# Kernel optimization log

Hardware: AMD Instinct MI355X
Metric: run time of the kernel (lower is better)

Reference implementation:

```python
import jax, jax.numpy as jnp
import numpy as np

V = 32000   # vocab
E = 512     # hidden_size (d_model)
NH = 8      # num_heads
DH = E // NH
NL = 2      # num_layers
FF = 2048   # TransformerDecoderLayer default dim_feedforward
MAXLEN = 24 # cfg.max_length -> gen_len (no target given)
S, B = 48, 8
TRANS = 14
INIT = TRANS - 2            # tgt = transform[1:-1]
LF = INIT + MAXLEN - 1      # final tgt length after the loop
EPS = 1e-5
NEG = -1e9


def pos_encoding(length, d):
    pos = np.arange(length, dtype=np.float32)[:, None]
    div = np.exp(-np.log(10000.0) * np.arange(0, d, 2, dtype=np.float32) / d)
    pe = np.zeros((length, d), dtype=np.float32)
    pe[:, 0::2] = np.sin(pos * div)
    pe[:, 1::2] = np.cos(pos * div)
    return jnp.asarray(pe)


def setup_inputs() -> dict:
    key = jax.random.key(0)
    ks = jax.random.split(key, 12)
    s = 0.02
    return {
        "enc_outputs": jax.random.normal(ks[0], (S, B, E), jnp.float32),
        "transform": jax.random.randint(ks[1], (TRANS, B), 0, V),
        "tf_ratio": 0,
        "emb_table": jax.random.normal(ks[2], (V, E), jnp.float32) * s,
        "sa_w": jax.random.normal(ks[3], (NL, 3 * E, E), jnp.float32) * s,
        "sa_b": jnp.zeros((NL, 3 * E), jnp.float32),
        "sa_ow": jax.random.normal(ks[4], (NL, E, E), jnp.float32) * s,
        "sa_ob": jnp.zeros((NL, E), jnp.float32),
        "ca_w": jax.random.normal(ks[5], (NL, 3 * E, E), jnp.float32) * s,
        "ca_b": jnp.zeros((NL, 3 * E), jnp.float32),
        "ca_ow": jax.random.normal(ks[6], (NL, E, E), jnp.float32) * s,
        "ca_ob": jnp.zeros((NL, E), jnp.float32),
        "ff1_w": jax.random.normal(ks[7], (NL, FF, E), jnp.float32) * s,
        "ff1_b": jnp.zeros((NL, FF), jnp.float32),
        "ff2_w": jax.random.normal(ks[8], (NL, E, FF), jnp.float32) * s,
        "ff2_b": jnp.zeros((NL, E), jnp.float32),
        "ln_g": jnp.ones((NL, 3, E), jnp.float32),
        "ln_b": jnp.zeros((NL, 3, E), jnp.float32),
        "out_w": jax.random.normal(ks[9], (V, E), jnp.float32) * s,
        "out_b": jnp.zeros((V,), jnp.float32),
    }


def _ln(x, g, b):
    m = jnp.mean(x, -1, keepdims=True)
    v = jnp.mean((x - m) ** 2, -1, keepdims=True)
    return (x - m) * jax.lax.rsqrt(v + EPS) * g + b


def _mha(q_in, kv_in, w, b, ow, ob, mask):
    # q_in [Lq,B,E], kv_in [Lk,B,E]; PyTorch packed in_proj [3E,E]
    wq, wk, wv = jnp.split(w, 3, 0)
    bq, bk, bv = jnp.split(b, 3, 0)
    proj = lambda x, wm, bm: (x @ wm.T + bm).reshape(x.shape[0], x.shape[1], NH, DH)
    q, k, v = proj(q_in, wq, bq), proj(kv_in, wk, bk), proj(kv_in, wv, bv)
    sc = jnp.einsum('qbhd,kbhd->bhqk', q, k) / np.sqrt(DH).astype(np.float32)
    if mask is not None:
        sc = sc + mask
    a = jax.nn.softmax(sc, -1)
    o = jnp.einsum('bhqk,kbhd->qbhd', a, v).reshape(q_in.shape[0], q_in.shape[1], E)
    return o @ ow.T + ob


def _decoder(x, mem, mask, p):
    # post-norm TransformerDecoderLayer: self-attn -> cross-attn -> relu FFN
    for l in range(NL):
        x = _ln(x + _mha(x, x, p['sa_w'][l], p['sa_b'][l], p['sa_ow'][l], p['sa_ob'][l], mask),
                p['ln_g'][l, 0], p['ln_b'][l, 0])
        x = _ln(x + _mha(x, mem, p['ca_w'][l], p['ca_b'][l], p['ca_ow'][l], p['ca_ob'][l], None),
                p['ln_g'][l, 1], p['ln_b'][l, 1])
        h = jax.nn.relu(x @ p['ff1_w'][l].T + p['ff1_b'][l]) @ p['ff2_w'][l].T + p['ff2_b'][l]
        x = _ln(x + h, p['ln_g'][l, 2], p['ln_b'][l, 2])
    return x


def reference(enc_outputs, transform, tf_ratio, emb_table, sa_w, sa_b, sa_ow, sa_ob,
              ca_w, ca_b, ca_ow, ca_ob, ff1_w, ff1_b, ff2_w, ff2_b, ln_g, ln_b,
              out_w, out_b):
    # tf_ratio == 0 -> no teacher forcing; gen_len = max_length (no target attr)
    p = dict(sa_w=sa_w, sa_b=sa_b, sa_ow=sa_ow, sa_ob=sa_ob, ca_w=ca_w, ca_b=ca_b,
             ca_ow=ca_ow, ca_ob=ca_ob, ff1_w=ff1_w, ff1_b=ff1_b, ff2_w=ff2_w,
             ff2_b=ff2_b, ln_g=ln_g, ln_b=ln_b)
    pe = pos_encoding(MAXLEN, E)
    # causal mask over the fixed-size buffer; padded (future) slots cannot
    # influence valid positions, so full-buffer passes == torch prefix passes.
    mask = jnp.where(jnp.tril(jnp.ones((LF, LF), bool)), 0.0, NEG)
    tgt0 = emb_table[transform[1:-1]] + pe[:INIT][:, None, :]   # [INIT,B,E]
    buf = jnp.zeros((LF, B, E), jnp.float32).at[:INIT].set(tgt0)

    def step(buf, i):
        h = _decoder(buf, enc_outputs, mask, p)
        pos = INIT - 1 + i                        # last valid position
        pred = jnp.argmax(h[pos] @ out_w.T + out_b, axis=-1)   # [B]
        # torch re-embeds the single predicted token -> PE position 0
        emb = emb_table[pred] + pe[0]
        return buf.at[pos + 1].set(emb), None

    buf, _ = jax.lax.scan(step, buf, jnp.arange(MAXLEN - 1))
    h = _decoder(buf, enc_outputs, mask, p)       # final loop iteration's pass
    return h @ out_w.T + out_b                    # dec_outputs [LF,B,V]
```

## Files before the change

### kernel.cpp

```cpp
#include <hip/hip_runtime.h>
#include <hip/hip_bf16.h>
#include <math.h>

#define V    32000
#define E    512
#define NH   8
#define DH   64
#define NL   2
#define FF   2048
#define MAXLEN 24
#define S    48
#define B    8
#define TRANS 14
#define INIT 12
#define LF   35

#define NB   256
#define NT   512

typedef float f4 __attribute__((ext_vector_type(4)));

__device__ inline float wsum(float v) {
#pragma unroll
  for (int off = 32; off; off >>= 1) v += __shfl_xor(v, off);
  return v;
}
__device__ inline float wmax(float v) {
#pragma unroll
  for (int off = 32; off; off >>= 1) v = fmaxf(v, __shfl_xor(v, off));
  return v;
}

__device__ inline float ldc(const float* p) {
  return __hip_atomic_load(p, __ATOMIC_RELAXED, __HIP_MEMORY_SCOPE_AGENT);
}
__device__ inline void stc(float* p, float v) {
  __hip_atomic_store(p, v, __ATOMIC_RELAXED, __HIP_MEMORY_SCOPE_AGENT);
}
__device__ inline float2 ldc8(const float* p) {
  union { unsigned long long u; float2 f; } c;
  c.u = __hip_atomic_load((const unsigned long long*)p, __ATOMIC_RELAXED, __HIP_MEMORY_SCOPE_AGENT);
  return c.f;
}
__device__ inline void stc8(float* p, float x, float y) {
  union { unsigned long long u; float f[2]; } c; c.f[0] = x; c.f[1] = y;
  __hip_atomic_store((unsigned long long*)p, c.u, __ATOMIC_RELAXED, __HIP_MEMORY_SCOPE_AGENT);
}
__device__ inline int ldci(const int* p) {
  return __hip_atomic_load(p, __ATOMIC_RELAXED, __HIP_MEMORY_SCOPE_AGENT);
}
__device__ inline void stci(int* p, int v) {
  __hip_atomic_store(p, v, __ATOMIC_RELAXED, __HIP_MEMORY_SCOPE_AGENT);
}

#define CMB(v, idx, ov, oi) do { if ((ov) > (v) || ((ov) == (v) && (oi) < (idx))) { (v) = (ov); (idx) = (oi); } } while (0)


__global__ void embed_init_k(const int* __restrict__ transform, const float* __restrict__ emb,
                             float* __restrict__ xbuf) {
  int t = blockIdx.x;
  int pos = t >> 3, b = t & 7;
  int tok = transform[(1 + pos) * B + b];
  for (int d = threadIdx.x; d < E; d += blockDim.x) {
    double div = exp(-log(10000.0) * (double)(d & ~1) / (double)E);
    double ang = (double)pos * div;
    float pe = (d & 1) ? (float)cos(ang) : (float)sin(ang);
    xbuf[(size_t)t * E + d] = emb[(size_t)tok * E + d] + pe;
  }
}

template <int K>
__global__ __launch_bounds__(256) void gemm_k(
    const float* __restrict__ x, const float* __restrict__ W, const float* __restrict__ bias,
    int ntok, int nout, int route, int relu,
    float* __restrict__ out0, float* __restrict__ out1, float* __restrict__ out2) {
  constexpr int K4 = K / 4;
  constexpr int J  = K / 256;
  __shared__ float4 xt[8][K4];
  const int tid = threadIdx.x;
  const int lane = tid & 63;
  const int o = blockIdx.x * 4 + (tid >> 6);

  float4 wr[J];
  if (o < nout) {
    const float4* Wr = (const float4*)(W + (size_t)o * K);
#pragma unroll
    for (int j = 0; j < J; ++j) wr[j] = Wr[lane + 64 * j];
  }

  const int ng = ntok >> 3;
  for (int g = 0; g < ng; ++g) {
    if (g) __syncthreads();
    const float4* xg = (const float4*)(x + (size_t)g * 8 * K);
    float4* xf = &xt[0][0];
    for (int i = tid; i < 8 * K4; i += 256) xf[i] = xg[i];
    __syncthreads();
    if (o < nout) {
      float acc[8] = {0, 0, 0, 0, 0, 0, 0, 0};
#pragma unroll
      for (int j = 0; j < J; ++j) {
        float4 w = wr[j];
#pragma unroll
        for (int tt = 0; tt < 8; ++tt) {
          float4 xv = xt[tt][lane + 64 * j];
          acc[tt] += w.x * xv.x + w.y * xv.y + w.z * xv.z + w.w * xv.w;
        }
      }
#pragma unroll
      for (int tt = 0; tt < 8; ++tt) acc[tt] = wsum(acc[tt]);
      if (lane == 0) {
        float bo = bias[o];
#pragma unroll
        for (int tt = 0; tt < 8; ++tt) {
          float v = acc[tt] + bo;
          if (relu) v = fmaxf(v, 0.f);
          int t = g * 8 + tt;
          if (route == 0) {
            out0[(size_t)t * nout + o] = v;
          } else if (route == 1) {
            if (o < E) out0[(size_t)t * E + o] = v;
            else if (o < 2 * E) out1[(size_t)t * E + (o - E)] = v;
            else out2[(size_t)t * E + (o - 2 * E)] = v;
          } else {
            if (o < E) out0[(size_t)t * E + o] = v;
            else out1[(size_t)t * E + (o - E)] = v;
          }
        }
      }
    }
  }
}

__global__ __launch_bounds__(256) void attn_k(
    const float* __restrict__ q, const float* __restrict__ Kc, const float* __restrict__ Vc,
    float* __restrict__ outp, int p0, int nq, int nk_fixed, int causal) {
  const int tid = threadIdx.x;
  const int lane = tid & 63;
  const int u = blockIdx.x * 4 + (tid >> 6);
  if (u >= nq * 64) return;
  const int qi = u >> 6;
  const int r = u & 63;
  const int b = r >> 3, h = r & 7;
  const int nk = causal ? (p0 + qi + 1) : nk_fixed;

  const size_t qoff = (size_t)(qi * B + b) * E + h * DH + lane;
  const float qv = q[qoff];

  float myscore = -INFINITY;
  for (int k = 0; k < nk; ++k) {
    float prod = qv * Kc[(size_t)(k * B + b) * E + h * DH + lane];
    prod = wsum(prod);
    if (lane == k) myscore = prod * 0.125f;
  }
  float m = wmax(myscore);
  float p = (lane < nk) ? expf(myscore - m) : 0.f;
  float denom = wsum(p);
  float a = p / denom;

  float oacc = 0.f;
  for (int k = 0; k < nk; ++k) {
    float ak = __shfl(a, k);
    oacc = fmaf(ak, Vc[(size_t)(k * B + b) * E + h * DH + lane], oacc);
  }
  outp[qoff] = oacc;
}

__global__ __launch_bounds__(256) void add_ln_k(
    const float* __restrict__ xa, const float* __restrict__ xb,
    const float* __restrict__ g, const float* __restrict__ beta,
    float* __restrict__ outp, int ntok) {
  const int tid = threadIdx.x, lane = tid & 63;
  const int t = blockIdx.x * 4 + (tid >> 6);
  if (t >= ntok) return;
  float v[8];
  float s = 0.f;
#pragma unroll
  for (int j = 0; j < 8; ++j) {
    int d = lane + 64 * j;
    v[j] = xa[(size_t)t * E + d] + xb[(size_t)t * E + d];
    s += v[j];
  }
  s = wsum(s);
  float mean = s * (1.f / 512.f);
  float d2 = 0.f;
#pragma unroll
  for (int j = 0; j < 8; ++j) { float dd = v[j] - mean; d2 += dd * dd; }
  d2 = wsum(d2);
  float inv = 1.f / sqrtf(d2 * (1.f / 512.f) + 1e-5f);
#pragma unroll
  for (int j = 0; j < 8; ++j) {
    int d = lane + 64 * j;
    outp[(size_t)t * E + d] = (v[j] - mean) * inv * g[d] + beta[d];
  }
}


__global__ __launch_bounds__(NT, 1) void decode_persist_k(
    const float* __restrict__ emb,
    const float* __restrict__ sa_w, const float* __restrict__ sa_b,
    const float* __restrict__ sa_ow, const float* __restrict__ sa_ob,
    const float* __restrict__ ca_w, const float* __restrict__ ca_b,
    const float* __restrict__ ca_ow, const float* __restrict__ ca_ob,
    const float* __restrict__ ff1_w, const float* __restrict__ ff1_b,
    const float* __restrict__ ff2_w, const float* __restrict__ ff2_b,
    const float* __restrict__ ln_g, const float* __restrict__ ln_b,
    const float* __restrict__ out_w, const float* __restrict__ out_b,
    float* __restrict__ kself, float* __restrict__ vself,
    const float* __restrict__ kcross, const float* __restrict__ vcross,
    float* __restrict__ x3buf, float* __restrict__ xstep, float* __restrict__ part,
    float* __restrict__ amaxbuf, float* __restrict__ outp, int* __restrict__ bar) {
  __shared__ __align__(16) float s_x[E];
  __shared__ __align__(16) float s_q[DH];
  __shared__ __align__(16) float s_att[DH];
  __shared__ __align__(16) float s_h[256];
  __shared__ __align__(16) float s_tile[8 * E];
  __shared__ float s_rv[NT];
  __shared__ int   s_ri[NT];
  __shared__ float s_r1[8], s_r2[8];
  __shared__ float s_pv[8][8];
  __shared__ int   s_pi[8][8];

  const int tid  = threadIdx.x;
  const int lane = tid & 63;
  const int wv   = tid >> 6;
  const int g4   = lane >> 2;
  const int s4   = lane & 3;
  const int bid  = blockIdx.x;
  const int b    = bid >> 3;
  const int j    = bid & 7;

  int cgen = 0;

  auto cl_sync = [&]() {
    ++cgen;
    __syncthreads();
    if (tid == 0) {
      __hip_atomic_fetch_add(&bar[b * 32], 1, __ATOMIC_RELAXED, __HIP_MEMORY_SCOPE_AGENT);
      while (ldci(&bar[b * 32]) < 8 * cgen) __builtin_amdgcn_s_sleep(2);
    }
    __syncthreads();
  };

  auto dot512 = [&](const float* Wrow, const float* xin) -> float {
    const f4* Wp = (const f4*)Wrow;
    const f4* Xp = (const f4*)xin;
    float acc = 0.f;
#pragma unroll
    for (int u = 0; u < 32; ++u) {
      int jj = s4 * 32 + ((u + s4) & 31);
      f4 w = Wp[jj], x = Xp[jj];
      acc += w.x * x.x + w.y * x.y + w.z * x.z + w.w * x.w;
    }
    acc += __shfl_xor(acc, 1);
    acc += __shfl_xor(acc, 2);
    return acc;
  };
  auto dot256 = [&](const float* Wseg, const float* xin) -> float {
    const f4* Wp = (const f4*)Wseg;
    const f4* Xp = (const f4*)xin;
    float acc = 0.f;
#pragma unroll
    for (int u = 0; u < 16; ++u) {
      int jj = s4 * 16 + ((u + s4) & 15);
      f4 w = Wp[jj], x = Xp[jj];
      acc += w.x * x.x + w.y * x.y + w.z * x.z + w.w * x.w;
    }
    acc += __shfl_xor(acc, 1);
    acc += __shfl_xor(acc, 2);
    return acc;
  };
  auto dot64 = [&](const float* Wseg, const float* xin) -> float {
    const f4* Wp = (const f4*)Wseg;
    const f4* Xp = (const f4*)xin;
    float acc = 0.f;
#pragma unroll
    for (int u = 0; u < 4; ++u) {
      int jj = s4 * 4 + ((u + s4) & 3);
      f4 w = Wp[jj], x = Xp[jj];
      acc += w.x * x.x + w.y * x.y + w.z * x.z + w.w * x.w;
    }
    acc += __shfl_xor(acc, 1);
    acc += __shfl_xor(acc, 2);
    return acc;
  };

  auto blockLN = [&](float val, const float* gg, const float* be, float* dst) {
    float s1 = wsum(val);
    if (lane == 0) s_r1[wv] = s1;
    __syncthreads();
    float m = 0.f;
#pragma unroll
    for (int w2 = 0; w2 < 8; ++w2) m += s_r1[w2];
    m *= (1.f / 512.f);
    float d = val - m;
    float s2 = wsum(d * d);
    if (lane == 0) s_r2[wv] = s2;
    __syncthreads();
    float var = 0.f;
#pragma unroll
    for (int w2 = 0; w2 < 8; ++w2) var += s_r2[w2];
    var *= (1.f / 512.f);
    float inv = 1.f / sqrtf(var + 1e-5f);
    dst[tid] = d * inv * gg[tid] + be[tid];
    __syncthreads();
  };

  auto attn1 = [&](const float* Kbase, const float* Vbase, int nk) {
    if (wv == 0) {
      float sc = -INFINITY;
      if (lane < nk) {
        const f4* Kr = (const f4*)(Kbase + ((size_t)lane * B + b) * E + j * DH);
        const f4* Qp = (const f4*)s_q;
        float a0 = 0.f;
#pragma unroll
        for (int u = 0; u < 16; ++u) {
          f4 kv = Kr[u], qv = Qp[u];
          a0 += kv.x * qv.x + kv.y * qv.y + kv.z * qv.z + kv.w * qv.w;
        }
        sc = a0 * 0.125f;
      }
      float m = wmax(sc);
      float e = (lane < nk) ? expf(sc - m) : 0.f;
      float den = wsum(e);
      float aa = e / den;
      float o = 0.f;
      for (int k2 = 0; k2 < nk; ++k2) {
        float ak = __shfl(aa, k2);
        o = fmaf(ak, Vbase[((size_t)k2 * B + b) * E + j * DH + lane], o);
      }
      s_att[lane] = o;
    }
    __syncthreads();
  };

  for (int i = 0; i < MAXLEN - 1; ++i) {
    const int p = INIT + i;

    if (bid < 64) {
      if (j == 0) {
        if (i > 0) {
          if (tid < 32) {
            while (ldci(&bar[(18 + tid) * 32]) < 8 * i) __builtin_amdgcn_s_sleep(4);
          }
          __syncthreads();
          if (tid < 256) {
            float2 pr = ldc8(&amaxbuf[(size_t)(tid * 8 + b) * 2]);
            s_rv[tid] = pr.x; s_ri[tid] = (int)pr.y;
          } else { s_rv[tid] = -INFINITY; s_ri[tid] = 0x7fffffff; }
          __syncthreads();
          for (int st2 = 128; st2; st2 >>= 1) {
            if (tid < st2) {
              float ov = s_rv[tid + st2]; int oi = s_ri[tid + st2];
              CMB(s_rv[tid], s_ri[tid], ov, oi);
            }
            __syncthreads();
          }
        } else {
          const float* row = outp + ((size_t)(INIT - 1) * B + b) * V;
          float bv = -INFINITY; int bi = 0x7fffffff;
          for (int j2 = tid; j2 < V / 2; j2 += NT) {
            float2 vv = ldc8(row + 2 * j2);
            CMB(bv, bi, vv.x, 2 * j2);
            CMB(bv, bi, vv.y, 2 * j2 + 1);
          }
          s_rv[tid] = bv; s_ri[tid] = bi;
          __syncthreads();
          for (int st2 = NT / 2; st2; st2 >>= 1) {
            if (tid < st2) {
              float ov = s_rv[tid + st2]; int oi = s_ri[tid + st2];
              CMB(s_rv[tid], s_ri[tid], ov, oi);
            }
            __syncthreads();
          }
        }
        const int tok = s_ri[0];
        if (tid < 256) {
          int d0 = tid * 2;
          float e0 = emb[(size_t)tok * E + d0];
          float e1 = emb[(size_t)tok * E + d0 + 1] + 1.0f;
          s_x[d0] = e0; s_x[d0 + 1] = e1;
          stc8(&xstep[(size_t)b * E + d0], e0, e1);
        }
        __syncthreads();
        if (tid == 0) stci(&bar[(10 + b) * 32], i + 1);
      } else {
        if (tid == 0) {
          while (ldci(&bar[(10 + b) * 32]) < i + 1) __builtin_amdgcn_s_sleep(4);
        }
        __syncthreads();
        if (tid < 256) {
          float2 vv = ldc8(&xstep[(size_t)b * E + tid * 2]);
          s_x[tid * 2] = vv.x; s_x[tid * 2 + 1] = vv.y;
        }
        __syncthreads();
      }

      for (int l = 0; l < NL; ++l) {
        for (int c = wv; c < 12; c += 8) {
          int r = c * 16 + g4;
          int sec = r >> 6, off = r & 63;
          int wr = sec * E + j * DH + off;
          float val = dot512(sa_w + ((size_t)l * 3 * E + wr) * E, s_x);
          if (s4 == 0) {
            val += sa_b[(size_t)l * 3 * E + wr];
            if (sec == 0) s_q[off] = val;
            else if (sec == 1) kself[((size_t)(l * LF + p) * B + b) * E + j * DH + off] = val;
            else               vself[((size_t)(l * LF + p) * B + b) * E + j * DH + off] = val;
          }
        }
        __syncthreads();
        attn1(kself + (size_t)l * LF * B * E, vself + (size_t)l * LF * B * E, p + 1);
        for (int ps = 0; ps < 4; ++ps) {
          int r = wv * 64 + ps * 16 + g4;
          float val = dot64(sa_ow + ((size_t)l * E + r) * E + j * DH, s_att);
          if (s4 == 0) stc(&part[(((size_t)(l * 3 + 0) * 8 + b) * 8 + j) * E + r], val);
        }
        cl_sync();
        {
          float val = s_x[tid] + sa_ob[(size_t)l * E + tid];
          const float* pb = part + ((size_t)(l * 3 + 0) * 8 + b) * 8 * E + tid;
#pragma unroll
          for (int jj = 0; jj < 8; ++jj) val += ldc(pb + jj * E);
          blockLN(val, ln_g + (size_t)(l * 3 + 0) * E, ln_b + (size_t)(l * 3 + 0) * E, s_x);
        }
        if (wv < 4) {
          int r = wv * 16 + g4;
          float val = dot512(ca_w + ((size_t)l * 3 * E + j * DH + r) * E, s_x);
          if (s4 == 0) s_q[r] = val + ca_b[(size_t)l * 3 * E + j * DH + r];
        }
        __syncthreads();
        attn1(kcross + (size_t)l * S * B * E, vcross + (size_t)l * S * B * E, S);
        for (int ps = 0; ps < 4; ++ps) {
          int r = wv * 64 + ps * 16 + g4;
          float val = dot64(ca_ow + ((size_t)l * E + r) * E + j * DH, s_att);
          if (s4 == 0) stc(&part[(((size_t)(l * 3 + 1) * 8 + b) * 8 + j) * E + r], val);
        }
        cl_sync();
        {
          float val = s_x[tid] + ca_ob[(size_t)l * E + tid];
          const float* pb = part + ((size_t)(l * 3 + 1) * 8 + b) * 8 * E + tid;
#pragma unroll
          for (int jj = 0; jj < 8; ++jj) val += ldc(pb + jj * E);
          blockLN(val, ln_g + (size_t)(l * 3 + 1) * E, ln_b + (size_t)(l * 3 + 1) * E, s_x);
        }
        for (int c = wv; c < 16; c += 8) {
          int r = c * 16 + g4;
          int wr = j * 256 + r;
          float val = dot512(ff1_w + ((size_t)l * FF + wr) * E, s_x);
          if (s4 == 0) s_h[r] = fmaxf(val + ff1_b[(size_t)l * FF + wr], 0.f);
        }
        __syncthreads();
        for (int ps = 0; ps < 4; ++ps) {
          int r = wv * 64 + ps * 16 + g4;
          float val = dot256(ff2_w + ((size_t)l * E + r) * FF + j * 256, s_h);
          if (s4 == 0) stc(&part[(((size_t)(l * 3 + 2) * 8 + b) * 8 + j) * E + r], val);
        }
        cl_sync();
        {
          float val = s_x[tid] + ff2_b[(size_t)l * E + tid];
          const float* pb = part + ((size_t)(l * 3 + 2) * 8 + b) * 8 * E + tid;
#pragma unroll
          for (int jj = 0; jj < 8; ++jj) val += ldc(pb + jj * E);
          blockLN(val, ln_g + (size_t)(l * 3 + 2) * E, ln_b + (size_t)(l * 3 + 2) * E, s_x);
        }
      }

      if (j == 0) {
        if (tid < 256) stc8(&x3buf[(size_t)b * E + tid * 2], s_x[tid * 2], s_x[tid * 2 + 1]);
        __syncthreads();
        if (tid == 0) {
          int old = __hip_atomic_fetch_add(&bar[8 * 32], 1, __ATOMIC_RELAXED, __HIP_MEMORY_SCOPE_AGENT);
          if (old == 8 * (i + 1) - 1) stci(&bar[9 * 32], i + 1);
        }
      }
    }

    if (tid == 0) {
      while (ldci(&bar[9 * 32]) < i + 1) __builtin_amdgcn_s_sleep(4);
    }
    __syncthreads();
    for (int j2 = tid; j2 < 4 * E; j2 += NT) {
      float2 vv = ldc8(x3buf + 2 * j2);
      s_tile[2 * j2] = vv.x; s_tile[2 * j2 + 1] = vv.y;
    }
    __syncthreads();

    {
      const int idx = wv * 16 + g4;
      const bool valid = idx < 125;
      const int r = bid * 125 + idx;
      float acc[8] = {0, 0, 0, 0, 0, 0, 0, 0};
      if (valid) {
        const f4* Wp = (const f4*)(out_w + (size_t)r * E);
        const f4* Xp = (const f4*)s_tile;
#pragma unroll 8
        for (int u = 0; u < 32; ++u) {
          int jj = s4 * 32 + ((u + s4) & 31);
          f4 w = __builtin_nontemporal_load(Wp + jj);
#pragma unroll
          for (int t = 0; t < 8; ++t) {
            f4 x = Xp[t * 128 + jj];
            acc[t] += w.x * x.x + w.y * x.y + w.z * x.z + w.w * x.w;
          }
        }
#pragma unroll
        for (int t = 0; t < 8; ++t) {
          acc[t] += __shfl_xor(acc[t], 1);
          acc[t] += __shfl_xor(acc[t], 2);
          acc[t] += out_b[r];
        }
        if (s4 == 0) {
#pragma unroll
          for (int t = 0; t < 8; ++t)
            stc(&outp[((size_t)p * B + t) * V + r], acc[t]);
        }
      }
#pragma unroll
      for (int t = 0; t < 8; ++t) {
        float v = valid ? acc[t] : -INFINITY;
        int ix = valid ? r : 0x7fffffff;
#pragma unroll
        for (int off = 1; off < 64; off <<= 1) {
          float ov = __shfl_xor(v, off); int oi = __shfl_xor(ix, off);
          CMB(v, ix, ov, oi);
        }
        if (lane == 0) { s_pv[wv][t] = v; s_pi[wv][t] = ix; }
      }
    }
    __syncthreads();
    if (wv == 0) {
      int t = lane & 7, w2 = lane >> 3;
      float v = s_pv[w2][t]; int ix = s_pi[w2][t];
#pragma unroll
      for (int off = 8; off < 64; off <<= 1) {
        float ov = __shfl_xor(v, off); int oi = __shfl_xor(ix, off);
        CMB(v, ix, ov, oi);
      }
      if (lane < 8) stc8(&amaxbuf[(size_t)(bid * 8 + lane) * 2], v, (float)ix);
    }
    __syncthreads();
    if (tid == 0)
      __hip_atomic_fetch_add(&bar[(18 + (bid & 31)) * 32], 1, __ATOMIC_RELAXED, __HIP_MEMORY_SCOPE_AGENT);
  }
}

extern "C" void kernel_launch(void* const* d_in, const int* in_sizes, int n_in,
                              void* d_out, int out_size, void* d_ws, size_t ws_size,
                              hipStream_t stream) {
  const float* enc       = (const float*)d_in[0];
  const int*   transform = (const int*)d_in[1];
  const float* emb       = (const float*)d_in[3];
  const float* sa_w  = (const float*)d_in[4];
  const float* sa_b  = (const float*)d_in[5];
  const float* sa_ow = (const float*)d_in[6];
  const float* sa_ob = (const float*)d_in[7];
  const float* ca_w  = (const float*)d_in[8];
  const float* ca_b  = (const float*)d_in[9];
  const float* ca_ow = (const float*)d_in[10];
  const float* ca_ob = (const float*)d_in[11];
  const float* ff1_w = (const float*)d_in[12];
  const float* ff1_b = (const float*)d_in[13];
  const float* ff2_w = (const float*)d_in[14];
  const float* ff2_b = (const float*)d_in[15];
  const float* ln_g  = (const float*)d_in[16];
  const float* ln_b  = (const float*)d_in[17];
  const float* out_w = (const float*)d_in[18];
  const float* out_b = (const float*)d_in[19];
  float* out = (float*)d_out;

  const size_t SELF_SZ  = (size_t)LF * B * E;
  const size_t CROSS_SZ = (size_t)S * B * E;
  float* ws     = (float*)d_ws;
  float* xbuf   = ws;
  float* kself  = xbuf + (size_t)INIT * B * E;
  float* vself  = kself + NL * SELF_SZ;
  float* kcross = vself + NL * SELF_SZ;
  float* vcross = kcross + NL * CROSS_SZ;
  float* act0   = vcross + NL * CROSS_SZ;
  float* act1   = act0 + 96 * E;
  float* act2   = act1 + 96 * E;
  float* act3   = act2 + 96 * E;
  float* ffb    = act3 + 96 * E;
  int*   bar    = (int*)(ffb + 96 * FF);

  float* x3buf  = act0;
  float* xstep  = act0 + 8 * E;
  float* amaxb  = act0 + 16 * E;
  float* partb  = ffb;

  hipMemsetAsync(bar, 0, 8192, stream);

  embed_init_k<<<INIT * B, 128, 0, stream>>>(transform, emb, xbuf);

  for (int l = 0; l < NL; ++l) {
    gemm_k<E><<<(2 * E) / 4, 256, 0, stream>>>(
        enc, ca_w + ((size_t)l * 3 * E + E) * E, ca_b + (size_t)l * 3 * E + E,
        S * B, 2 * E, 2, 0, kcross + l * CROSS_SZ, vcross + l * CROSS_SZ, nullptr);
  }

  {
    const int p0 = 0, nq = INIT, ntok = nq * B;
    const float* xin = xbuf;
    for (int l = 0; l < NL; ++l) {
      const float* x = (l == 0) ? xin : act1;
      gemm_k<E><<<(3 * E) / 4, 256, 0, stream>>>(
          x, sa_w + (size_t)l * 3 * E * E, sa_b + (size_t)l * 3 * E, ntok, 3 * E, 1, 0,
          act2, kself + l * SELF_SZ, vself + l * SELF_SZ);
      attn_k<<<nq * 16, 256, 0, stream>>>(act2, kself + l * SELF_SZ, vself + l * SELF_SZ,
                                          act3, p0, nq, 0, 1);
      gemm_k<E><<<E / 4, 256, 0, stream>>>(
          act3, sa_ow + (size_t)l * E * E, sa_ob + (size_t)l * E, ntok, E, 0, 0, act2, nullptr, nullptr);
      add_ln_k<<<(ntok + 3) / 4, 256, 0, stream>>>(
          x, act2, ln_g + (size_t)l * 3 * E, ln_b + (size_t)l * 3 * E, act1, ntok);
      gemm_k<E><<<E / 4, 256, 0, stream>>>(
          act1, ca_w + (size_t)l * 3 * E * E, ca_b + (size_t)l * 3 * E, ntok, E, 0, 0, act2, nullptr, nullptr);
      attn_k<<<nq * 16, 256, 0, stream>>>(act2, kcross + l * CROSS_SZ, vcross + l * CROSS_SZ,
                                          act3, p0, nq, S, 0);
      gemm_k<E><<<E / 4, 256, 0, stream>>>(
          act3, ca_ow + (size_t)l * E * E, ca_ob + (size_t)l * E, ntok, E, 0, 0, act2, nullptr, nullptr);
      add_ln_k<<<(ntok + 3) / 4, 256, 0, stream>>>(
          act1, act2, ln_g + (size_t)l * 3 * E + E, ln_b + (size_t)l * 3 * E + E, act1, ntok);
      gemm_k<E><<<FF / 4, 256, 0, stream>>>(
          act1, ff1_w + (size_t)l * FF * E, ff1_b + (size_t)l * FF, ntok, FF, 0, 1, ffb, nullptr, nullptr);
      gemm_k<FF><<<E / 4, 256, 0, stream>>>(
          ffb, ff2_w + (size_t)l * E * FF, ff2_b + (size_t)l * E, ntok, E, 0, 0, act2, nullptr, nullptr);
      add_ln_k<<<(ntok + 3) / 4, 256, 0, stream>>>(
          act1, act2, ln_g + (size_t)l * 3 * E + 2 * E, ln_b + (size_t)l * 3 * E + 2 * E, act1, ntok);
    }
    gemm_k<E><<<V / 4, 256, 0, stream>>>(
        act1, out_w, out_b, ntok, V, 0, 0, out, nullptr, nullptr);
  }

  decode_persist_k<<<NB, NT, 0, stream>>>(
      emb, sa_w, sa_b, sa_ow, sa_ob, ca_w, ca_b, ca_ow, ca_ob,
      ff1_w, ff1_b, ff2_w, ff2_b, ln_g, ln_b, out_w, out_b,
      kself, vself, kcross, vcross, x3buf, xstep, partb, amaxb, out, bar);
}
```

Baseline: 5.299 ms.

## Keep decoder weights resident in LDS across all blocks with grid barriers

Before the decode loop, each of the 256 persistent blocks copies its slice of every decoder-layer weight matrix (QKV, self-out, cross-Q, cross-out, FF1, FF2) into shared memory once. The per-step decoder then spreads each projection across all blocks, joined by a hierarchical grid barrier. Previously 64 blocks re-read the weights from global memory on every step and used per-batch cluster syncs. The vocab projection now loads out_w through inline-asm nontemporal cache-bypass loads. The trade-off is many more grid-wide barriers per step, plus extra global round trips for activations between stages, and an LDS footprint close to the per-CU limit.

```diff
diff --git a/kernel.cpp b/kernel.cpp
--- a/kernel.cpp
+++ b/kernel.cpp
@@ -49,8 +49,21 @@
 __device__ inline int ldci(const int* p) {
   return __hip_atomic_load(p, __ATOMIC_RELAXED, __HIP_MEMORY_SCOPE_AGENT);
 }
-__device__ inline void stci(int* p, int v) {
-  __hip_atomic_store(p, v, __ATOMIC_RELAXED, __HIP_MEMORY_SCOPE_AGENT);
+
+__device__ inline void ld8_bypass(const float* p, f4* w) {
+  asm volatile(
+      "global_load_dwordx4 %0, %8, off sc0 sc1 nt\n\t"
+      "global_load_dwordx4 %1, %8, off offset:16 sc0 sc1 nt\n\t"
+      "global_load_dwordx4 %2, %8, off offset:32 sc0 sc1 nt\n\t"
+      "global_load_dwordx4 %3, %8, off offset:48 sc0 sc1 nt\n\t"
+      "global_load_dwordx4 %4, %8, off offset:64 sc0 sc1 nt\n\t"
+      "global_load_dwordx4 %5, %8, off offset:80 sc0 sc1 nt\n\t"
+      "global_load_dwordx4 %6, %8, off offset:96 sc0 sc1 nt\n\t"
+      "global_load_dwordx4 %7, %8, off offset:112 sc0 sc1 nt\n\t"
+      "s_waitcnt vmcnt(0)"
+      : "=&v"(w[0]), "=&v"(w[1]), "=&v"(w[2]), "=&v"(w[3]),
+        "=&v"(w[4]), "=&v"(w[5]), "=&v"(w[6]), "=&v"(w[7])
+      : "v"(p));
 }
 
 #define CMB(v, idx, ov, oi) do { if ((ov) > (v) || ((ov) == (v) && (oi) < (idx))) { (v) = (ov); (idx) = (oi); } } while (0)
@@ -194,6 +207,13 @@
   }
 }
 
+#define B_QKV 0
+#define B_OW  6144
+#define B_CQ  8192
+#define B_COW 10240
+#define B_FF1 12288
+#define B_FF2 20480
+#define SW_TOT 28672
 
 __global__ __launch_bounds__(NT, 1) void decode_persist_k(
     const float* __restrict__ emb,
@@ -207,16 +227,17 @@
     const float* __restrict__ out_w, const float* __restrict__ out_b,
     float* __restrict__ kself, float* __restrict__ vself,
     const float* __restrict__ kcross, const float* __restrict__ vcross,
-    float* __restrict__ x3buf, float* __restrict__ xstep, float* __restrict__ part,
-    float* __restrict__ amaxbuf, float* __restrict__ outp, int* __restrict__ bar) {
-  __shared__ __align__(16) float s_x[E];
-  __shared__ __align__(16) float s_q[DH];
-  __shared__ __align__(16) float s_att[DH];
-  __shared__ __align__(16) float s_h[256];
-  __shared__ __align__(16) float s_tile[8 * E];
+    float* __restrict__ xstep, float* __restrict__ qbuf, float* __restrict__ attbuf,
+    float* __restrict__ rawbuf, float* __restrict__ x1buf, float* __restrict__ x2buf,
+    float* __restrict__ x3buf, float* __restrict__ ybuf, float* __restrict__ hbuf,
+    float* __restrict__ pbuf, float* __restrict__ amaxbuf,
+    float* __restrict__ outp, int* __restrict__ bar) {
+  __shared__ __align__(16) float s_w[SW_TOT];
+  __shared__ __align__(16) float s_x[8 * E];
+  __shared__ __align__(16) float s_y[8 * E];
+  __shared__ __align__(16) float s_q2[64];
   __shared__ float s_rv[NT];
   __shared__ int   s_ri[NT];
-  __shared__ float s_r1[8], s_r2[8];
   __shared__ float s_pv[8][8];
   __shared__ int   s_pi[8][8];
 
@@ -226,91 +247,82 @@
   const int g4   = lane >> 2;
   const int s4   = lane & 3;
   const int bid  = blockIdx.x;
-  const int b    = bid >> 3;
-  const int j    = bid & 7;
-
-  int cgen = 0;
-
-  auto cl_sync = [&]() {
-    ++cgen;
+  int gen = 0;
+
+  auto gbar = [&]() {
+    ++gen;
     __syncthreads();
-    if (tid == 0) {
-      __hip_atomic_fetch_add(&bar[b * 32], 1, __ATOMIC_RELAXED, __HIP_MEMORY_SCOPE_AGENT);
-      while (ldci(&bar[b * 32]) < 8 * cgen) __builtin_amdgcn_s_sleep(2);
+    if (tid == 0)
+      __hip_atomic_fetch_add(&bar[(bid & 31) * 32], 1, __ATOMIC_RELAXED, __HIP_MEMORY_SCOPE_AGENT);
+    if (wv == 0) {
+      const int target = gen * 8;
+      for (;;) {
+        int c = ldci(&bar[(lane & 31) * 32]);
+        if (__all(c >= target)) break;
+        __builtin_amdgcn_s_sleep(2);
+      }
     }
     __syncthreads();
   };
 
-  auto dot512 = [&](const float* Wrow, const float* xin) -> float {
-    const f4* Wp = (const f4*)Wrow;
-    const f4* Xp = (const f4*)xin;
-    float acc = 0.f;
-#pragma unroll
-    for (int u = 0; u < 32; ++u) {
-      int jj = s4 * 32 + ((u + s4) & 31);
-      f4 w = Wp[jj], x = Xp[jj];
-      acc += w.x * x.x + w.y * x.y + w.z * x.z + w.w * x.w;
-    }
-    acc += __shfl_xor(acc, 1);
-    acc += __shfl_xor(acc, 2);
-    return acc;
+  auto stage_in = [&](float* dst, const float* src) {
+    for (int k = tid; k < 2048; k += NT) {
+      float2 vv = ldc8(src + 2 * k);
+      dst[2 * k] = vv.x; dst[2 * k + 1] = vv.y;
+    }
   };
-  auto dot256 = [&](const float* Wseg, const float* xin) -> float {
-    const f4* Wp = (const f4*)Wseg;
-    const f4* Xp = (const f4*)xin;
-    float acc = 0.f;
-#pragma unroll
-    for (int u = 0; u < 16; ++u) {
-      int jj = s4 * 16 + ((u + s4) & 15);
-      f4 w = Wp[jj], x = Xp[jj];
-      acc += w.x * x.x + w.y * x.y + w.z * x.z + w.w * x.w;
-    }
-    acc += __shfl_xor(acc, 1);
-    acc += __shfl_xor(acc, 2);
-    return acc;
-  };
-  auto dot64 = [&](const float* Wseg, const float* xin) -> float {
-    const f4* Wp = (const f4*)Wseg;
-    const f4* Xp = (const f4*)xin;
-    float acc = 0.f;
-#pragma unroll
-    for (int u = 0; u < 4; ++u) {
-      int jj = s4 * 4 + ((u + s4) & 3);
-      f4 w = Wp[jj], x = Xp[jj];
-      acc += w.x * x.x + w.y * x.y + w.z * x.z + w.w * x.w;
-    }
-    acc += __shfl_xor(acc, 1);
-    acc += __shfl_xor(acc, 2);
-    return acc;
-  };
-
-  auto blockLN = [&](float val, const float* gg, const float* be, float* dst) {
-    float s1 = wsum(val);
-    if (lane == 0) s_r1[wv] = s1;
-    __syncthreads();
-    float m = 0.f;
-#pragma unroll
-    for (int w2 = 0; w2 < 8; ++w2) m += s_r1[w2];
-    m *= (1.f / 512.f);
-    float d = val - m;
-    float s2 = wsum(d * d);
-    if (lane == 0) s_r2[wv] = s2;
-    __syncthreads();
-    float var = 0.f;
-#pragma unroll
-    for (int w2 = 0; w2 < 8; ++w2) var += s_r2[w2];
-    var *= (1.f / 512.f);
-    float inv = 1.f / sqrtf(var + 1e-5f);
-    dst[tid] = d * inv * gg[tid] + be[tid];
+  auto lnstage = [&](int lnidx) {
+    const float* gg = ln_g + (size_t)lnidx * E;
+    const float* be = ln_b + (size_t)lnidx * E;
+    float v[8]; float sum = 0.f;
+#pragma unroll
+    for (int j = 0; j < 8; ++j) {
+      int d = lane + 64 * j;
+      v[j] = s_x[wv * E + d] + s_y[wv * E + d];
+      sum += v[j];
+    }
+    sum = wsum(sum);
+    float mean = sum * (1.f / 512.f);
+    float d2 = 0.f;
+#pragma unroll
+    for (int j = 0; j < 8; ++j) { float dd = v[j] - mean; d2 += dd * dd; }
+    d2 = wsum(d2);
+    float inv = 1.f / sqrtf(d2 * (1.f / 512.f) + 1e-5f);
+#pragma unroll
+    for (int j = 0; j < 8; ++j) {
+      int d = lane + 64 * j;
+      s_x[wv * E + d] = (v[j] - mean) * inv * gg[d] + be[d];
+    }
     __syncthreads();
   };
-
-  auto attn1 = [&](const float* Kbase, const float* Vbase, int nk) {
+  auto publish = [&](float* dst) {
+    for (int k = tid; k < 256; k += NT)
+      stc8(&dst[bid * E + 2 * k], s_x[bid * E + 2 * k], s_x[bid * E + 2 * k + 1]);
+  };
+  auto proj2 = [&](int wbase, const float* biasp, float* dst) {
+    const int row = wv & 1;
+    const int r = bid * 2 + row;
+    const f4* wp = (const f4*)&s_w[wbase + row * 512];
+    f4 w0 = wp[lane], w1 = wp[lane + 64];
+    float bias = biasp[r];
+#pragma unroll
+    for (int half = 0; half < 2; ++half) {
+      int b = (wv >> 1) + half * 4;
+      const f4* x4 = (const f4*)&s_x[b * E];
+      f4 a = w0 * x4[lane] + w1 * x4[lane + 64];
+      float acc = a.x + a.y + a.z + a.w;
+      acc = wsum(acc);
+      if (lane == 0) stc(&dst[b * E + r], acc + bias);
+    }
+  };
+  auto attn_stage = [&](const float* Kbase, const float* Vbase, int nk) {
+    const int b = bid >> 3, h = bid & 7;
     if (wv == 0) {
+      s_q2[lane] = ldc(&qbuf[b * E + h * DH + lane]);
       float sc = -INFINITY;
       if (lane < nk) {
-        const f4* Kr = (const f4*)(Kbase + ((size_t)lane * B + b) * E + j * DH);
-        const f4* Qp = (const f4*)s_q;
+        const f4* Kr = (const f4*)(Kbase + ((size_t)lane * B + b) * E + h * DH);
+        const f4* Qp = (const f4*)s_q2;
         float a0 = 0.f;
 #pragma unroll
         for (int u = 0; u < 16; ++u) {
@@ -323,224 +335,243 @@
       float e = (lane < nk) ? expf(sc - m) : 0.f;
       float den = wsum(e);
       float aa = e / den;
-      float o = 0.f;
+      float oa = 0.f;
+#pragma unroll 4
       for (int k2 = 0; k2 < nk; ++k2) {
         float ak = __shfl(aa, k2);
-        o = fmaf(ak, Vbase[((size_t)k2 * B + b) * E + j * DH + lane], o);
-      }
-      s_att[lane] = o;
+        oa = fmaf(ak, Vbase[((size_t)k2 * B + b) * E + h * DH + lane], oa);
+      }
+      stc(&attbuf[b * E + h * DH + lane], oa);
+    }
+  };
+
+  {
+    auto cprow = [&](const float* src, int dstf) {
+      f4* d = (f4*)&s_w[dstf];
+      const f4* s = (const f4*)src;
+      for (int k = tid; k < 128; k += NT) d[k] = s[k];
+    };
+    const int kc = bid >> 6;
+    for (int l = 0; l < NL; ++l) {
+      for (int j = 0; j < 6; ++j)
+        cprow(sa_w + ((size_t)l * 1536 + bid * 6 + j) * E, B_QKV + (l * 6 + j) * 512);
+      for (int j = 0; j < 2; ++j) {
+        cprow(sa_ow + ((size_t)l * 512 + bid * 2 + j) * E, B_OW + (l * 2 + j) * 512);
+        cprow(ca_w + ((size_t)l * 1536 + bid * 2 + j) * E, B_CQ + (l * 2 + j) * 512);
+        cprow(ca_ow + ((size_t)l * 512 + bid * 2 + j) * E, B_COW + (l * 2 + j) * 512);
+      }
+      for (int j = 0; j < 8; ++j) {
+        cprow(ff1_w + ((size_t)l * FF + bid * 8 + j) * E, B_FF1 + (l * 8 + j) * 512);
+        cprow(ff2_w + ((size_t)l * 512 + (bid & 63) * 8 + j) * FF + kc * 512,
+              B_FF2 + (l * 8 + j) * 512);
+      }
     }
     __syncthreads();
-  };
+  }
 
   for (int i = 0; i < MAXLEN - 1; ++i) {
     const int p = INIT + i;
 
-    if (bid < 64) {
-      if (j == 0) {
-        if (i > 0) {
-          if (tid < 32) {
-            while (ldci(&bar[(18 + tid) * 32]) < 8 * i) __builtin_amdgcn_s_sleep(4);
+    if (bid < 8) {
+      const int b = bid;
+      if (i == 0) {
+        const float* row = outp + ((size_t)(INIT - 1) * B + b) * V;
+        float bv = -INFINITY; int bi = 0x7fffffff;
+        for (int j2 = tid; j2 < V / 2; j2 += NT) {
+          float2 vv = ldc8(row + 2 * j2);
+          CMB(bv, bi, vv.x, 2 * j2);
+          CMB(bv, bi, vv.y, 2 * j2 + 1);
+        }
+        s_rv[tid] = bv; s_ri[tid] = bi;
+      } else {
+        if (tid < 256) {
+          float2 pr = ldc8(&amaxbuf[(size_t)(tid * 8 + b) * 2]);
+          s_rv[tid] = pr.x; s_ri[tid] = (int)pr.y;
+        } else { s_rv[tid] = -INFINITY; s_ri[tid] = 0x7fffffff; }
+      }
+      __syncthreads();
+      for (int st2 = NT / 2; st2; st2 >>= 1) {
+        if (tid < st2) {
+          float ov = s_rv[tid + st2]; int oi = s_ri[tid + st2];
+          CMB(s_rv[tid], s_ri[tid], ov, oi);
+        }
+        __syncthreads();
+      }
+      const int tok = s_ri[0];
+      if (tid < 256) {
+        int d0 = tid * 2;
+        float e0 = emb[(size_t)tok * E + d0];
+        float e1 = emb[(size_t)tok * E + d0 + 1] + 1.0f;
+        stc8(&xstep[(size_t)b * E + d0], e0, e1);
+      }
+    }
+    gbar();
+
+    for (int l = 0; l < NL; ++l) {
+      if (l == 0) {
+        stage_in(s_x, xstep);
+        __syncthreads();
+      } else {
+        stage_in(s_x, x2buf); stage_in(s_y, ybuf);
+        __syncthreads();
+        lnstage(2);
+        if (bid < 8) publish(x3buf);
+      }
+      if (wv < 6) {
+        const int r = bid * 6 + wv;
+        const int sec = r >> 9, off = r & 511;
+        const f4* wp = (const f4*)&s_w[B_QKV + (l * 6 + wv) * 512];
+        f4 w0 = wp[lane], w1 = wp[lane + 64];
+        float bias = sa_b[(size_t)l * 1536 + r];
+#pragma unroll
+        for (int b = 0; b < 8; ++b) {
+          const f4* x4 = (const f4*)&s_x[b * E];
+          f4 a = w0 * x4[lane] + w1 * x4[lane + 64];
+          float acc = a.x + a.y + a.z + a.w;
+          acc = wsum(acc);
+          if (lane == 0) {
+            acc += bias;
+            if (sec == 0) stc(&qbuf[b * E + off], acc);
+            else if (sec == 1) stc(&kself[((size_t)(l * LF + p) * B + b) * E + off], acc);
+            else stc(&vself[((size_t)(l * LF + p) * B + b) * E + off], acc);
           }
-          __syncthreads();
-          if (tid < 256) {
-            float2 pr = ldc8(&amaxbuf[(size_t)(tid * 8 + b) * 2]);
-            s_rv[tid] = pr.x; s_ri[tid] = (int)pr.y;
-          } else { s_rv[tid] = -INFINITY; s_ri[tid] = 0x7fffffff; }
-          __syncthreads();
-          for (int st2 = 128; st2; st2 >>= 1) {
-            if (tid < st2) {
-              float ov = s_rv[tid + st2]; int oi = s_ri[tid + st2];
-              CMB(s_rv[tid], s_ri[tid], ov, oi);
-            }
-            __syncthreads();
+        }
+      }
+      gbar();
+      if (bid < 64) attn_stage(kself + (size_t)l * LF * B * E, vself + (size_t)l * LF * B * E, p + 1);
+      gbar();
+      stage_in(s_x, attbuf);
+      __syncthreads();
+      proj2(B_OW + l * 1024, sa_ob + (size_t)l * 512, rawbuf);
+      gbar();
+      stage_in(s_x, (l == 0) ? xstep : x3buf); stage_in(s_y, rawbuf);
+      __syncthreads();
+      lnstage(l * 3 + 0);
+      if (bid < 8) publish(x1buf);
+      proj2(B_CQ + l * 1024, ca_b + (size_t)l * 1536, qbuf);
+      gbar();
+      if (bid < 64) attn_stage(kcross + (size_t)l * S * B * E, vcross + (size_t)l * S * B * E, S);
+      gbar();
+      stage_in(s_x, attbuf);
+      __syncthreads();
+      proj2(B_COW + l * 1024, ca_ob + (size_t)l * 512, rawbuf);
+      gbar();
+      stage_in(s_x, x1buf); stage_in(s_y, rawbuf);
+      __syncthreads();
+      lnstage(l * 3 + 1);
+      if (bid < 8) publish(x2buf);
+      {
+        const int r = bid * 8 + wv;
+        const f4* wp = (const f4*)&s_w[B_FF1 + (l * 8 + wv) * 512];
+        f4 w0 = wp[lane], w1 = wp[lane + 64];
+        float bias = ff1_b[(size_t)l * FF + r];
+#pragma unroll
+        for (int b = 0; b < 8; ++b) {
+          const f4* x4 = (const f4*)&s_x[b * E];
+          f4 a = w0 * x4[lane] + w1 * x4[lane + 64];
+          float acc = a.x + a.y + a.z + a.w;
+          acc = wsum(acc);
+          if (lane == 0) stc(&hbuf[b * FF + r], fmaxf(acc + bias, 0.f));
+        }
+      }
+      gbar();
+      {
+        const int kc = bid >> 6;
+        for (int k = tid; k < 2048; k += NT) {
+          int b = k >> 8, d2 = (k & 255) * 2;
+          float2 vv = ldc8(&hbuf[b * FF + kc * 512 + d2]);
+          s_x[b * E + d2] = vv.x; s_x[b * E + d2 + 1] = vv.y;
+        }
+        __syncthreads();
+        const int rowf = (bid & 63) * 8 + wv;
+        const f4* wp = (const f4*)&s_w[B_FF2 + (l * 8 + wv) * 512];
+        f4 w0 = wp[lane], w1 = wp[lane + 64];
+#pragma unroll
+        for (int b = 0; b < 8; ++b) {
+          const f4* x4 = (const f4*)&s_x[b * E];
+          f4 a = w0 * x4[lane] + w1 * x4[lane + 64];
+          float acc = a.x + a.y + a.z + a.w;
+          acc = wsum(acc);
+          if (lane == 0) stc(&pbuf[(size_t)(kc * 512 + rowf) * 8 + b], acc);
+        }
+      }
+      gbar();
+      {
+        const int row = bid * 2 + (wv & 1);
+#pragma unroll
+        for (int half = 0; half < 2; ++half) {
+          int b = (wv >> 1) + half * 4;
+          if (lane == 0) {
+            float y = ff2_b[(size_t)l * 512 + row];
+#pragma unroll
+            for (int kc = 0; kc < 4; ++kc) y += ldc(&pbuf[(size_t)(kc * 512 + row) * 8 + b]);
+            stc(&ybuf[b * E + row], y);
           }
-        } else {
-          const float* row = outp + ((size_t)(INIT - 1) * B + b) * V;
-          float bv = -INFINITY; int bi = 0x7fffffff;
-          for (int j2 = tid; j2 < V / 2; j2 += NT) {
-            float2 vv = ldc8(row + 2 * j2);
-            CMB(bv, bi, vv.x, 2 * j2);
-            CMB(bv, bi, vv.y, 2 * j2 + 1);
-          }
-          s_rv[tid] = bv; s_ri[tid] = bi;
-          __syncthreads();
-          for (int st2 = NT / 2; st2; st2 >>= 1) {
-            if (tid < st2) {
-              float ov = s_rv[tid + st2]; int oi = s_ri[tid + st2];
-              CMB(s_rv[tid], s_ri[tid], ov, oi);
-            }
-            __syncthreads();
-          }
-        }
-        const int tok = s_ri[0];
-        if (tid < 256) {
-          int d0 = tid * 2;
-          float e0 = emb[(size_t)tok * E + d0];
-          float e1 = emb[(size_t)tok * E + d0 + 1] + 1.0f;
-          s_x[d0] = e0; s_x[d0 + 1] = e1;
-          stc8(&xstep[(size_t)b * E + d0], e0, e1);
-        }
-        __syncthreads();
-        if (tid == 0) stci(&bar[(10 + b) * 32], i + 1);
-      } else {
-        if (tid == 0) {
-          while (ldci(&bar[(10 + b) * 32]) < i + 1) __builtin_amdgcn_s_sleep(4);
-        }
-        __syncthreads();
-        if (tid < 256) {
-          float2 vv = ldc8(&xstep[(size_t)b * E + tid * 2]);
-          s_x[tid * 2] = vv.x; s_x[tid * 2 + 1] = vv.y;
-        }
-        __syncthreads();
-      }
-
-      for (int l = 0; l < NL; ++l) {
-        for (int c = wv; c < 12; c += 8) {
-          int r = c * 16 + g4;
-          int sec = r >> 6, off = r & 63;
-          int wr = sec * E + j * DH + off;
-          float val = dot512(sa_w + ((size_t)l * 3 * E + wr) * E, s_x);
-          if (s4 == 0) {
-            val += sa_b[(size_t)l * 3 * E + wr];
-            if (sec == 0) s_q[off] = val;
-            else if (sec == 1) kself[((size_t)(l * LF + p) * B + b) * E + j * DH + off] = val;
-            else               vself[((size_t)(l * LF + p) * B + b) * E + j * DH + off] = val;
-          }
-        }
-        __syncthreads();
-        attn1(kself + (size_t)l * LF * B * E, vself + (size_t)l * LF * B * E, p + 1);
-        for (int ps = 0; ps < 4; ++ps) {
-          int r = wv * 64 + ps * 16 + g4;
-          float val = dot64(sa_ow + ((size_t)l * E + r) * E + j * DH, s_att);
-          if (s4 == 0) stc(&part[(((size_t)(l * 3 + 0) * 8 + b) * 8 + j) * E + r], val);
-        }
-        cl_sync();
-        {
-          float val = s_x[tid] + sa_ob[(size_t)l * E + tid];
-          const float* pb = part + ((size_t)(l * 3 + 0) * 8 + b) * 8 * E + tid;
-#pragma unroll
-          for (int jj = 0; jj < 8; ++jj) val += ldc(pb + jj * E);
-          blockLN(val, ln_g + (size_t)(l * 3 + 0) * E, ln_b + (size_t)(l * 3 + 0) * E, s_x);
-        }
-        if (wv < 4) {
-          int r = wv * 16 + g4;
-          float val = dot512(ca_w + ((size_t)l * 3 * E + j * DH + r) * E, s_x);
-          if (s4 == 0) s_q[r] = val + ca_b[(size_t)l * 3 * E + j * DH + r];
-        }
-        __syncthreads();
-        attn1(kcross + (size_t)l * S * B * E, vcross + (size_t)l * S * B * E, S);
-        for (int ps = 0; ps < 4; ++ps) {
-          int r = wv * 64 + ps * 16 + g4;
-          float val = dot64(ca_ow + ((size_t)l * E + r) * E + j * DH, s_att);
-          if (s4 == 0) stc(&part[(((size_t)(l * 3 + 1) * 8 + b) * 8 + j) * E + r], val);
-        }
-        cl_sync();
-        {
-          float val = s_x[tid] + ca_ob[(size_t)l * E + tid];
-          const float* pb = part + ((size_t)(l * 3 + 1) * 8 + b) * 8 * E + tid;
-#pragma unroll
-          for (int jj = 0; jj < 8; ++jj) val += ldc(pb + jj * E);
-          blockLN(val, ln_g + (size_t)(l * 3 + 1) * E, ln_b + (size_t)(l * 3 + 1) * E, s_x);
-        }
-        for (int c = wv; c < 16; c += 8) {
-          int r = c * 16 + g4;
-          int wr = j * 256 + r;
-          float val = dot512(ff1_w + ((size_t)l * FF + wr) * E, s_x);
-          if (s4 == 0) s_h[r] = fmaxf(val + ff1_b[(size_t)l * FF + wr], 0.f);
-        }
-        __syncthreads();
-        for (int ps = 0; ps < 4; ++ps) {
-          int r = wv * 64 + ps * 16 + g4;
-          float val = dot256(ff2_w + ((size_t)l * E + r) * FF + j * 256, s_h);
-          if (s4 == 0) stc(&part[(((size_t)(l * 3 + 2) * 8 + b) * 8 + j) * E + r], val);
-        }
-        cl_sync();
-        {
-          float val = s_x[tid] + ff2_b[(size_t)l * E + tid];
-          const float* pb = part + ((size_t)(l * 3 + 2) * 8 + b) * 8 * E + tid;
-#pragma unroll
-          for (int jj = 0; jj < 8; ++jj) val += ldc(pb + jj * E);
-          blockLN(val, ln_g + (size_t)(l * 3 + 2) * E, ln_b + (size_t)(l * 3 + 2) * E, s_x);
-        }
-      }
-
-      if (j == 0) {
-        if (tid < 256) stc8(&x3buf[(size_t)b * E + tid * 2], s_x[tid * 2], s_x[tid * 2 + 1]);
-        __syncthreads();
-        if (tid == 0) {
-          int old = __hip_atomic_fetch_add(&bar[8 * 32], 1, __ATOMIC_RELAXED, __HIP_MEMORY_SCOPE_AGENT);
-          if (old == 8 * (i + 1) - 1) stci(&bar[9 * 32], i + 1);
-        }
-      }
-    }
-
-    if (tid == 0) {
-      while (ldci(&bar[9 * 32]) < i + 1) __builtin_amdgcn_s_sleep(4);
-    }
+        }
+      }
+      gbar();
+    }
+
+    stage_in(s_x, x2buf); stage_in(s_y, ybuf);
     __syncthreads();
-    for (int j2 = tid; j2 < 4 * E; j2 += NT) {
-      float2 vv = ldc8(x3buf + 2 * j2);
-      s_tile[2 * j2] = vv.x; s_tile[2 * j2 + 1] = vv.y;
-    }
-    __syncthreads();
-
+    lnstage(5);
     {
       const int idx = wv * 16 + g4;
       const bool valid = idx < 125;
       const int r = bid * 125 + idx;
       float acc[8] = {0, 0, 0, 0, 0, 0, 0, 0};
       if (valid) {
-        const f4* Wp = (const f4*)(out_w + (size_t)r * E);
-        const f4* Xp = (const f4*)s_tile;
-#pragma unroll 8
-        for (int u = 0; u < 32; ++u) {
-          int jj = s4 * 32 + ((u + s4) & 31);
-          f4 w = __builtin_nontemporal_load(Wp + jj);
-#pragma unroll
-          for (int t = 0; t < 8; ++t) {
-            f4 x = Xp[t * 128 + jj];
-            acc[t] += w.x * x.x + w.y * x.y + w.z * x.z + w.w * x.w;
+        const float* wrow = out_w + (size_t)r * E + s4 * 128;
+#pragma unroll
+        for (int seg = 0; seg < 4; ++seg) {
+          f4 w8[8];
+          ld8_bypass(wrow + seg * 32, w8);
+#pragma unroll
+          for (int b = 0; b < 8; ++b) {
+            const f4* x4 = (const f4*)&s_x[b * E + s4 * 128 + seg * 32];
+#pragma unroll
+            for (int q = 0; q < 8; ++q) {
+              f4 xx = x4[q];
+              acc[b] += w8[q].x * xx.x + w8[q].y * xx.y + w8[q].z * xx.z + w8[q].w * xx.w;
+            }
           }
         }
 #pragma unroll
-        for (int t = 0; t < 8; ++t) {
-          acc[t] += __shfl_xor(acc[t], 1);
-          acc[t] += __shfl_xor(acc[t], 2);
-          acc[t] += out_b[r];
+        for (int b = 0; b < 8; ++b) {
+          acc[b] += __shfl_xor(acc[b], 1);
+          acc[b] += __shfl_xor(acc[b], 2);
+          acc[b] += out_b[r];
         }
         if (s4 == 0) {
 #pragma unroll
-          for (int t = 0; t < 8; ++t)
-            stc(&outp[((size_t)p * B + t) * V + r], acc[t]);
-        }
-      }
-#pragma unroll
-      for (int t = 0; t < 8; ++t) {
-        float v = valid ? acc[t] : -INFINITY;
+          for (int b = 0; b < 8; ++b)
+            stc(&outp[((size_t)p * B + b) * V + r], acc[b]);
+        }
+      }
+#pragma unroll
+      for (int b = 0; b < 8; ++b) {
+        float v = valid ? acc[b] : -INFINITY;
         int ix = valid ? r : 0x7fffffff;
 #pragma unroll
         for (int off = 1; off < 64; off <<= 1) {
           float ov = __shfl_xor(v, off); int oi = __shfl_xor(ix, off);
           CMB(v, ix, ov, oi);
         }
-        if (lane == 0) { s_pv[wv][t] = v; s_pi[wv][t] = ix; }
-      }
-    }
-    __syncthreads();
-    if (wv == 0) {
-      int t = lane & 7, w2 = lane >> 3;
-      float v = s_pv[w2][t]; int ix = s_pi[w2][t];
-#pragma unroll
-      for (int off = 8; off < 64; off <<= 1) {
-        float ov = __shfl_xor(v, off); int oi = __shfl_xor(ix, off);
-        CMB(v, ix, ov, oi);
-      }
-      if (lane < 8) stc8(&amaxbuf[(size_t)(bid * 8 + lane) * 2], v, (float)ix);
-    }
-    __syncthreads();
-    if (tid == 0)
-      __hip_atomic_fetch_add(&bar[(18 + (bid & 31)) * 32], 1, __ATOMIC_RELAXED, __HIP_MEMORY_SCOPE_AGENT);
+        if (lane == 0) { s_pv[wv][b] = v; s_pi[wv][b] = ix; }
+      }
+      __syncthreads();
+      if (wv == 0) {
+        int b = lane & 7, w2 = lane >> 3;
+        float v = s_pv[w2][b]; int ix = s_pi[w2][b];
+#pragma unroll
+        for (int off = 8; off < 64; off <<= 1) {
+          float ov = __shfl_xor(v, off); int oi = __shfl_xor(ix, off);
+          CMB(v, ix, ov, oi);
+        }
+        if (lane < 8) stc8(&amaxbuf[(size_t)(bid * 8 + lane) * 2], v, (float)ix);
+      }
+    }
+    gbar();
   }
 }
 
@@ -576,19 +607,24 @@
   float* vself  = kself + NL * SELF_SZ;
   float* kcross = vself + NL * SELF_SZ;
   float* vcross = kcross + NL * CROSS_SZ;
-  float* act0   = vcross + NL * CROSS_SZ;
-  float* act1   = act0 + 96 * E;
+  float* xstep  = vcross + NL * CROSS_SZ;
+  float* qbuf   = xstep + 8 * E;
+  float* attbuf = qbuf + 8 * E;
+  float* rawbuf = attbuf + 8 * E;
+  float* x1buf  = rawbuf + 8 * E;
+  float* x2buf  = x1buf + 8 * E;
+  float* x3buf  = x2buf + 8 * E;
+  float* ybuf   = x3buf + 8 * E;
+  float* hbuf   = ybuf + 8 * E;
+  float* pbuf   = hbuf + 8 * FF;
+  float* amaxb  = pbuf + 4 * 512 * 8;
+  int*   bar    = (int*)(amaxb + 256 * 8 * 2);
+  float* act1   = (float*)(bar + 1024);
   float* act2   = act1 + 96 * E;
   float* act3   = act2 + 96 * E;
   float* ffb    = act3 + 96 * E;
-  int*   bar    = (int*)(ffb + 96 * FF);
-
-  float* x3buf  = act0;
-  float* xstep  = act0 + 8 * E;
-  float* amaxb  = act0 + 16 * E;
-  float* partb  = ffb;
-
-  hipMemsetAsync(bar, 0, 8192, stream);
+
+  hipMemsetAsync(bar, 0, 4096, stream);
 
   embed_init_k<<<INIT * B, 128, 0, stream>>>(transform, emb, xbuf);
 
@@ -634,5 +670,7 @@
   decode_persist_k<<<NB, NT, 0, stream>>>(
       emb, sa_w, sa_b, sa_ow, sa_ob, ca_w, ca_b, ca_ow, ca_ob,
       ff1_w, ff1_b, ff2_w, ff2_b, ln_g, ln_b, out_w, out_b,
-      kself, vself, kcross, vcross, x3buf, xstep, partb, amaxb, out, bar);
-}
+      kself, vself, kcross, vcross,
+      xstep, qbuf, attbuf, rawbuf, x1buf, x2buf, x3buf, ybuf, hbuf, pbuf, amaxb,
+      out, bar);
+}
```

Result: slower. 5.523 ms (+4.2%).
